# Performance work log

Measured on AMD Instinct MI355X. Metric: run time of the kernel, lower is better.

Reference implementation:

```python
import jax, jax.numpy as jnp
import numpy as np

B, T, D = 16, 2048, 256
QK = 64


def setup_inputs() -> dict:
    key = jax.random.key(0)
    ks = jax.random.split(key, 9)
    x = jax.random.normal(ks[0], (B, T, D), dtype=jnp.float32)
    sl = jax.random.uniform(ks[1], (B, T), dtype=jnp.float32)
    mask = jax.random.randint(ks[2], (B, T), 0, 2, dtype=jnp.int32)
    s = 1.0 / np.sqrt(D).astype(np.float32)
    Wq = jax.random.normal(ks[3], (QK, D), dtype=jnp.float32) * s
    bq = jnp.zeros((QK,), dtype=jnp.float32)
    Wk = jax.random.normal(ks[4], (QK, D), dtype=jnp.float32) * s
    bk = jnp.zeros((QK,), dtype=jnp.float32)
    Wv = jax.random.normal(ks[5], (D, D), dtype=jnp.float32) * s
    bv = jnp.zeros((D,), dtype=jnp.float32)
    return {"x": x, "sl": sl, "mask": mask, "Wq": Wq, "bq": bq,
            "Wk": Wk, "bk": bk, "Wv": Wv, "bv": bv}


def reference(x, sl, mask, Wq, bq, Wk, bk, Wv, bv):
    # x: [B,T,D], sl: [B,T] soft labels, mask: [B,T] valid positions
    sl = jnp.clip(sl, 0.0, 1.0)
    q = jnp.einsum('btd,ed->bte', x, Wq) + bq          # [B,T,QK]
    k = jnp.einsum('btd,ed->bte', x, Wk) + bk          # [B,T,QK]
    v = jnp.einsum('btd,ed->bte', x, Wv) + bv          # [B,T,D]
    scale = jnp.float32(1.0 / np.sqrt(QK))
    score = jnp.einsum('bte,bse->bts', q, k) * scale   # [B,T,T]
    # emotion scaling by (1 + sl_j^2) per key position j
    score = score * (1.0 + sl[:, None, :] ** 2)
    score = jnp.where(mask[:, None, :] == 0, jnp.float32(-1e9), score)
    prob = jax.nn.softmax(score, axis=-1)              # [B,T,T]
    out = jnp.einsum('bts,bsd->btd', prob, v)          # [B,T,D]
    return out.mean(axis=1)                            # [B,D]
```

## Files before the change

kernel.cpp:

```cpp
#include <hip/hip_runtime.h>
#include <hip/hip_bf16.h>
#include <stdint.h>

#define B_ 16
#define T_ 2048
#define D_ 256
#define QK_ 64
#define LOG2E 1.44269504088896340736f

typedef _Float16 f16;
typedef _Float16 f16x8 __attribute__((ext_vector_type(8)));
typedef float f32x16 __attribute__((ext_vector_type(16)));

__device__ __forceinline__ void gload_lds16(const void* g, void* l) {
    __builtin_amdgcn_global_load_lds(
        (const __attribute__((address_space(1))) uint32_t*)g,
        (__attribute__((address_space(3))) uint32_t*)l, 16, 0, 0);
}

__device__ __forceinline__ float fexp2(float x) {
#if __has_builtin(__builtin_amdgcn_exp2f)
    return __builtin_amdgcn_exp2f(x);
#else
    return exp2f(x);
#endif
}
__device__ __forceinline__ float flog2(float x) {
#if __has_builtin(__builtin_amdgcn_logf)
    return __builtin_amdgcn_logf(x);
#else
    return log2f(x);
#endif
}

__global__ __launch_bounds__(256) void wconv_kernel(
    const float* __restrict__ Wq, const float* __restrict__ Wk,
    f16* __restrict__ wh)
{
    const int i = blockIdx.x * 256 + threadIdx.x;
    const float v = (i < 64 * 256) ? Wq[i] : Wk[i - 64 * 256];
    wh[i] = (f16)v;
}

__global__ __launch_bounds__(256) void proj_mfma(
    const float* __restrict__ x, const float* __restrict__ sl,
    const f16* __restrict__ wh,
    const float* __restrict__ bq, const float* __restrict__ bk,
    f16* __restrict__ qh, f16* __restrict__ k2h)
{
    __shared__ __align__(16) f16 xs[64 * D_];
    __shared__ float ksc[64];
    const int b = blockIdx.y, t0 = blockIdx.x * 64;
    const int tid = threadIdx.x;
    const int wv = tid >> 6, l = tid & 63, lo = l & 31, hi = l >> 5;

    #pragma unroll
    for (int i = 0; i < 8; ++i) {
        const int f = i * 256 + tid;
        const int r = f >> 5, j = f & 31;
        const float* src = x + ((size_t)b * T_ + t0 + r) * D_ + j * 8;
        const float4 a0 = *(const float4*)src;
        const float4 a1 = *(const float4*)(src + 4);
        f16x8 h;
        h[0] = (f16)a0.x; h[1] = (f16)a0.y; h[2] = (f16)a0.z; h[3] = (f16)a0.w;
        h[4] = (f16)a1.x; h[5] = (f16)a1.y; h[6] = (f16)a1.z; h[7] = (f16)a1.w;
        *(f16x8*)(xs + r * D_ + ((j ^ (r & 31)) << 3)) = h;
    }
    if (tid < 64) {
        float s = sl[(size_t)b * T_ + t0 + tid];
        s = fminf(fmaxf(s, 0.f), 1.f);
        ksc[tid] = 0.125f * (1.f + s * s) * LOG2E;
    }
    __syncthreads();

    const int r0 = (wv & 1) * 32, c0 = (wv >> 1) * 64;
    f32x16 acc0, acc1;
    #pragma unroll
    for (int i = 0; i < 16; ++i) { acc0[i] = 0.f; acc1[i] = 0.f; }

    const int r = r0 + lo;
    const f16* wrow0 = wh + (size_t)(c0 + lo) * D_ + hi * 8;
    const f16* wrow1 = wh + (size_t)(c0 + 32 + lo) * D_ + hi * 8;
    #pragma unroll
    for (int ks = 0; ks < 16; ++ks) {
        const f16x8 a  = *(const f16x8*)(xs + r * D_ + ((((ks << 1) + hi) ^ (r & 31)) << 3));
        const f16x8 b0 = *(const f16x8*)(wrow0 + ks * 16);
        const f16x8 b1 = *(const f16x8*)(wrow1 + ks * 16);
        acc0 = __builtin_amdgcn_mfma_f32_32x32x16_f16(a, b0, acc0, 0, 0, 0);
        acc1 = __builtin_amdgcn_mfma_f32_32x32x16_f16(a, b1, acc1, 0, 0, 0);
    }

    __syncthreads();
    f16* hout = xs;
    {
        const int col0 = c0 + lo, col1 = c0 + 32 + lo;
        const float bias0 = (col0 < 64) ? bq[col0] : bk[col0 - 64];
        const float bias1 = (col1 < 64) ? bq[col1] : bk[col1 - 64];
        #pragma unroll
        for (int i = 0; i < 16; ++i) {
            const int row = r0 + (i & 3) + 8 * (i >> 2) + 4 * hi;
            float v0 = acc0[i] + bias0;
            float v1 = acc1[i] + bias1;
            if (col0 >= 64) v0 *= ksc[row];
            if (col1 >= 64) v1 *= ksc[row];
            hout[row * 128 + col0] = (f16)v0;
            hout[row * 128 + col1] = (f16)v1;
        }
    }
    __syncthreads();
    #pragma unroll
    for (int i = 0; i < 4; ++i) {
        const int f = i * 256 + tid;
        const int rr = f >> 4, j = f & 15;
        const f16x8 v = *(const f16x8*)(hout + rr * 128 + j * 8);
        if (j < 8) *(f16x8*)(qh  + ((size_t)b * T_ + t0 + rr) * QK_ + j * 8) = v;
        else       *(f16x8*)(k2h + ((size_t)b * T_ + t0 + rr) * QK_ + (j - 8) * 8) = v;
    }
}

__global__ __launch_bounds__(256) void z_part(
    const f16* __restrict__ qh, const f16* __restrict__ k2h,
    const int* __restrict__ mask, float* __restrict__ zpart)
{
    __shared__ __align__(16) f16 kt[2][128 * QK_];
    __shared__ float mv[2][128];
    const int b = blockIdx.y;
    const int t0 = (blockIdx.x & 15) * 128;
    const int ck = blockIdx.x >> 4;
    const int sbase = ck * 512;
    const int tid = threadIdx.x;
    const int wv = tid >> 6, l = tid & 63, lo = l & 31, hi = l >> 5;

    const f16* qrow = qh + (size_t)(b * T_ + t0 + wv * 32 + lo) * QK_;
    f16x8 a[4];
    #pragma unroll
    for (int kc = 0; kc < 4; ++kc)
        a[kc] = *(const f16x8*)(qrow + kc * 16 + hi * 8);

    float zp[16];
    #pragma unroll
    for (int i = 0; i < 16; ++i) zp[i] = 0.f;

    auto stage = [&](int s0, int buf) {
        const char* src = (const char*)(k2h + (size_t)(b * T_ + s0) * QK_);
        #pragma unroll
        for (int i = 0; i < 4; ++i) {
            const int o = wv * 4096 + i * 1024 + l * 16;
            const int r = o >> 7, jc = (o >> 4) & 7;
            gload_lds16(src + r * 128 + ((jc ^ (r & 7)) << 4),
                        (char*)kt[buf] + wv * 4096 + i * 1024);
        }
        if (tid < 128) mv[buf][tid] = mask[b * T_ + s0 + tid] ? 0.f : -1e9f;
    };

    stage(sbase, 0);
    __syncthreads();
    int cur = 0;
    #pragma unroll
    for (int it = 0; it < 4; ++it) {
        if (it + 1 < 4) stage(sbase + (it + 1) * 128, cur ^ 1);
        const f16* ktc = kt[cur];
        #pragma unroll
        for (int cg = 0; cg < 4; ++cg) {
            const int srow = cg * 32 + lo;
            const float mb = mv[cur][srow];
            f32x16 c;
            #pragma unroll
            for (int i = 0; i < 16; ++i) c[i] = mb;
            #pragma unroll
            for (int kc = 0; kc < 4; ++kc) {
                const int jcc = (kc * 2 + hi) ^ (srow & 7);
                const f16x8 bf = *(const f16x8*)((const char*)ktc + srow * 128 + (jcc << 4));
                c = __builtin_amdgcn_mfma_f32_32x32x16_f16(a[kc], bf, c, 0, 0, 0);
            }
            #pragma unroll
            for (int i = 0; i < 16; ++i) zp[i] += fexp2(c[i]);
        }
        __syncthreads();
        cur ^= 1;
    }

    #pragma unroll
    for (int off = 1; off <= 16; off <<= 1)
        #pragma unroll
        for (int i = 0; i < 16; ++i) zp[i] += __shfl_xor(zp[i], off);

    if (lo == 0) {
        #pragma unroll
        for (int i = 0; i < 16; ++i) {
            const int row = (i & 3) + 8 * (i >> 2) + 4 * hi;
            zpart[(size_t)(b * 4 + ck) * T_ + t0 + wv * 32 + row] = zp[i];
        }
    }
}

__global__ __launch_bounds__(256) void w_part(
    const f16* __restrict__ qh, const f16* __restrict__ k2h,
    const float* __restrict__ zpart, float* __restrict__ wpart)
{
    __shared__ __align__(16) f16 qt[2][128 * QK_];
    __shared__ float lz[2][128];
    const int b = blockIdx.y;
    const int s0b = (blockIdx.x & 15) * 128;
    const int tc = blockIdx.x >> 4;
    const int tbase = tc * 512;
    const int tid = threadIdx.x;
    const int wv = tid >> 6, l = tid & 63, lo = l & 31, hi = l >> 5;

    const f16* krow = k2h + (size_t)(b * T_ + s0b + wv * 32 + lo) * QK_;
    f16x8 a[4];
    #pragma unroll
    for (int kc = 0; kc < 4; ++kc)
        a[kc] = *(const f16x8*)(krow + kc * 16 + hi * 8);

    float wp[16];
    #pragma unroll
    for (int i = 0; i < 16; ++i) wp[i] = 0.f;

    auto stage = [&](int t0, int buf) {
        const char* src = (const char*)(qh + (size_t)(b * T_ + t0) * QK_);
        #pragma unroll
        for (int i = 0; i < 4; ++i) {
            const int o = wv * 4096 + i * 1024 + l * 16;
            const int r = o >> 7, jc = (o >> 4) & 7;
            gload_lds16(src + r * 128 + ((jc ^ (r & 7)) << 4),
                        (char*)qt[buf] + wv * 4096 + i * 1024);
        }
        if (tid < 128) {
            const float z = zpart[(size_t)(b * 4 + 0) * T_ + t0 + tid]
                          + zpart[(size_t)(b * 4 + 1) * T_ + t0 + tid]
                          + zpart[(size_t)(b * 4 + 2) * T_ + t0 + tid]
                          + zpart[(size_t)(b * 4 + 3) * T_ + t0 + tid];
            lz[buf][tid] = -flog2(z);
        }
    };

    stage(tbase, 0);
    __syncthreads();
    int cur = 0;
    #pragma unroll
    for (int it = 0; it < 4; ++it) {
        if (it + 1 < 4) stage(tbase + (it + 1) * 128, cur ^ 1);
        const f16* qtc = qt[cur];
        #pragma unroll
        for (int cg = 0; cg < 4; ++cg) {
            const int trow = cg * 32 + lo;
            const float bias = lz[cur][trow];
            f32x16 c;
            #pragma unroll
            for (int i = 0; i < 16; ++i) c[i] = bias;
            #pragma unroll
            for (int kc = 0; kc < 4; ++kc) {
                const int jcc = (kc * 2 + hi) ^ (trow & 7);
                const f16x8 bf = *(const f16x8*)((const char*)qtc + trow * 128 + (jcc << 4));
                c = __builtin_amdgcn_mfma_f32_32x32x16_f16(a[kc], bf, c, 0, 0, 0);
            }
            #pragma unroll
            for (int i = 0; i < 16; ++i) wp[i] += fexp2(c[i]);
        }
        __syncthreads();
        cur ^= 1;
    }

    #pragma unroll
    for (int off = 1; off <= 16; off <<= 1)
        #pragma unroll
        for (int i = 0; i < 16; ++i) wp[i] += __shfl_xor(wp[i], off);

    if (lo == 0) {
        #pragma unroll
        for (int i = 0; i < 16; ++i) {
            const int row = (i & 3) + 8 * (i >> 2) + 4 * hi;
            wpart[(size_t)(b * 4 + tc) * T_ + s0b + wv * 32 + row] = wp[i];
        }
    }
}

__global__ __launch_bounds__(256) void y_fused(
    const float* __restrict__ x, const float* __restrict__ wpart,
    const int* __restrict__ mask, float* __restrict__ ypart,
    float* __restrict__ swp)
{
    __shared__ float wloc[32];
    const int b  = blockIdx.y;
    const int ch = blockIdx.x;
    const int tid = threadIdx.x;

    if (tid < 32) {
        const int s = ch * 32 + tid;
        float v = wpart[(size_t)(b * 4 + 0) * T_ + s]
                + wpart[(size_t)(b * 4 + 1) * T_ + s]
                + wpart[(size_t)(b * 4 + 2) * T_ + s]
                + wpart[(size_t)(b * 4 + 3) * T_ + s];
        v *= mask[b * T_ + s] ? (1.f / (float)T_) : 0.f;
        wloc[tid] = v;
        float sv = v;
        #pragma unroll
        for (int off = 1; off <= 16; off <<= 1) sv += __shfl_xor(sv, off);
        if (tid == 0) swp[b * 64 + ch] = sv;
    }
    __syncthreads();

    const int d = tid;
    const float* xb = x + ((size_t)b * T_ + ch * 32) * D_;
    float acc = 0.f;
    #pragma unroll 8
    for (int s = 0; s < 32; ++s) acc += wloc[s] * xb[(size_t)s * D_ + d];
    ypart[((size_t)b * 64 + ch) * D_ + d] = acc;
}

__global__ __launch_bounds__(256) void outkernel(
    const float* __restrict__ ypart, const float* __restrict__ swp,
    const float* __restrict__ Wv, const float* __restrict__ bv,
    float* __restrict__ out)
{
    __shared__ __align__(16) float ys[D_];
    __shared__ float sw0;
    const int b   = blockIdx.x;
    const int tid = threadIdx.x;

    float yv = 0.f;
    #pragma unroll
    for (int ch = 0; ch < 64; ++ch) yv += ypart[((size_t)b * 64 + ch) * D_ + tid];
    ys[tid] = yv;

    float s = (tid < 64) ? swp[b * 64 + tid] : 0.f;
    #pragma unroll
    for (int off = 1; off <= 32; off <<= 1) s += __shfl_xor(s, off);
    if (tid == 0) sw0 = s;
    __syncthreads();

    const float sw = sw0;
    const float4* wv4 = (const float4*)(Wv + (size_t)tid * D_);
    const float4* ys4 = (const float4*)ys;
    float o = 0.f;
    for (int i = 0; i < D_ / 4; ++i) {
        const float4 a = wv4[i];
        const float4 y = ys4[i];
        o += a.x * y.x + a.y * y.y + a.z * y.z + a.w * y.w;
    }
    out[(size_t)b * D_ + tid] = o + bv[tid] * sw;
}

extern "C" void kernel_launch(void* const* d_in, const int* in_sizes, int n_in,
                              void* d_out, int out_size, void* d_ws, size_t ws_size,
                              hipStream_t stream)
{
    const float* x    = (const float*)d_in[0];
    const float* sl   = (const float*)d_in[1];
    const int*   mask = (const int*)d_in[2];
    const float* Wq   = (const float*)d_in[3];
    const float* bq   = (const float*)d_in[4];
    const float* Wk   = (const float*)d_in[5];
    const float* bk   = (const float*)d_in[6];
    const float* Wv   = (const float*)d_in[7];
    const float* bv   = (const float*)d_in[8];
    float* out = (float*)d_out;

    f16*   qh    = (f16*)d_ws;
    f16*   k2h   = qh + (size_t)B_ * T_ * QK_;
    f16*   wh    = k2h + (size_t)B_ * T_ * QK_;
    float* zpart = (float*)(wh + 128 * D_);
    float* wpart = zpart + (size_t)B_ * 4 * T_;
    float* swp   = wpart + (size_t)B_ * 4 * T_;
    float* yp    = swp + B_ * 64;

    wconv_kernel<<<dim3(128), 256, 0, stream>>>(Wq, Wk, wh);
    proj_mfma  <<<dim3(T_ / 64, B_), 256, 0, stream>>>(x, sl, wh, bq, bk, qh, k2h);
    z_part     <<<dim3(64, B_), 256, 0, stream>>>(qh, k2h, mask, zpart);
    w_part     <<<dim3(64, B_), 256, 0, stream>>>(qh, k2h, zpart, wpart);
    y_fused    <<<dim3(64, B_), 256, 0, stream>>>(x, wpart, mask, yp, swp);
    outkernel  <<<dim3(B_), 256, 0, stream>>>(yp, swp, Wv, bv, out);
}
```

Measured before the change: 81.31 us.

## Drop LDS staging in projection and score kernels, load operands directly from global

The projection kernel now handles 32 rows per block. Each wave loads its x rows from global memory, converts them to fp16 with packed conversion, and feeds them straight into MFMA, so the shared-memory x tile and one barrier are gone. The z_part and w_part kernels drop their double-buffered LDS staging of K/Q tiles and mask/normaliser values. Each lane now reads its B-operand rows and mask/log-sum values directly from global (L2-cached) memory, which removes the barriers and LDS traffic. The cost is more redundant global loads per wave and more reliance on cache hits, and the projection grid doubles in size.

```diff
diff --git a/kernel.cpp b/kernel.cpp
--- a/kernel.cpp
+++ b/kernel.cpp
@@ -9,14 +9,10 @@
 #define LOG2E 1.44269504088896340736f
 
 typedef _Float16 f16;
+typedef _Float16 f16x2 __attribute__((ext_vector_type(2)));
+typedef __fp16 fp16x2 __attribute__((ext_vector_type(2)));
 typedef _Float16 f16x8 __attribute__((ext_vector_type(8)));
 typedef float f32x16 __attribute__((ext_vector_type(16)));
-
-__device__ __forceinline__ void gload_lds16(const void* g, void* l) {
-    __builtin_amdgcn_global_load_lds(
-        (const __attribute__((address_space(1))) uint32_t*)g,
-        (__attribute__((address_space(3))) uint32_t*)l, 16, 0, 0);
-}
 
 __device__ __forceinline__ float fexp2(float x) {
 #if __has_builtin(__builtin_amdgcn_exp2f)
@@ -32,6 +28,14 @@
     return log2f(x);
 #endif
 }
+__device__ __forceinline__ f16x2 cvt2(float a, float b) {
+#if __has_builtin(__builtin_amdgcn_cvt_pkrtz)
+    fp16x2 r = __builtin_amdgcn_cvt_pkrtz(a, b);
+    return __builtin_bit_cast(f16x2, r);
+#else
+    f16x2 r; r[0] = (f16)a; r[1] = (f16)b; return r;
+#endif
+}
 
 __global__ __launch_bounds__(256) void wconv_kernel(
     const float* __restrict__ Wq, const float* __restrict__ Wk,
@@ -48,73 +52,55 @@
     const float* __restrict__ bq, const float* __restrict__ bk,
     f16* __restrict__ qh, f16* __restrict__ k2h)
 {
-    __shared__ __align__(16) f16 xs[64 * D_];
-    __shared__ float ksc[64];
-    const int b = blockIdx.y, t0 = blockIdx.x * 64;
+    __shared__ __align__(16) f16 hout[32 * 128];
+    __shared__ float ksc[32];
+    const int b = blockIdx.y, t0 = blockIdx.x * 32;
     const int tid = threadIdx.x;
     const int wv = tid >> 6, l = tid & 63, lo = l & 31, hi = l >> 5;
 
-    #pragma unroll
-    for (int i = 0; i < 8; ++i) {
-        const int f = i * 256 + tid;
-        const int r = f >> 5, j = f & 31;
-        const float* src = x + ((size_t)b * T_ + t0 + r) * D_ + j * 8;
-        const float4 a0 = *(const float4*)src;
-        const float4 a1 = *(const float4*)(src + 4);
-        f16x8 h;
-        h[0] = (f16)a0.x; h[1] = (f16)a0.y; h[2] = (f16)a0.z; h[3] = (f16)a0.w;
-        h[4] = (f16)a1.x; h[5] = (f16)a1.y; h[6] = (f16)a1.z; h[7] = (f16)a1.w;
-        *(f16x8*)(xs + r * D_ + ((j ^ (r & 31)) << 3)) = h;
-    }
-    if (tid < 64) {
+    if (tid < 32) {
         float s = sl[(size_t)b * T_ + t0 + tid];
         s = fminf(fmaxf(s, 0.f), 1.f);
         ksc[tid] = 0.125f * (1.f + s * s) * LOG2E;
     }
+
+    const int c0 = wv * 32;
+    const float* xrow = x + (size_t)(b * T_ + t0 + lo) * D_ + hi * 8;
+    const f16*  wrow  = wh + (size_t)(c0 + lo) * D_ + hi * 8;
+
+    f32x16 acc;
+    #pragma unroll
+    for (int i = 0; i < 16; ++i) acc[i] = 0.f;
+
+    #pragma unroll
+    for (int ks = 0; ks < 16; ++ks) {
+        const float4 a0 = *(const float4*)(xrow + ks * 16);
+        const float4 a1 = *(const float4*)(xrow + ks * 16 + 4);
+        union { f16x2 h2[4]; f16x8 h8; } u;
+        u.h2[0] = cvt2(a0.x, a0.y); u.h2[1] = cvt2(a0.z, a0.w);
+        u.h2[2] = cvt2(a1.x, a1.y); u.h2[3] = cvt2(a1.z, a1.w);
+        const f16x8 bf = *(const f16x8*)(wrow + ks * 16);
+        acc = __builtin_amdgcn_mfma_f32_32x32x16_f16(u.h8, bf, acc, 0, 0, 0);
+    }
+
+    const int e = c0 + lo;
+    const float bias = (e < 64) ? bq[e] : bk[e - 64];
     __syncthreads();
-
-    const int r0 = (wv & 1) * 32, c0 = (wv >> 1) * 64;
-    f32x16 acc0, acc1;
-    #pragma unroll
-    for (int i = 0; i < 16; ++i) { acc0[i] = 0.f; acc1[i] = 0.f; }
-
-    const int r = r0 + lo;
-    const f16* wrow0 = wh + (size_t)(c0 + lo) * D_ + hi * 8;
-    const f16* wrow1 = wh + (size_t)(c0 + 32 + lo) * D_ + hi * 8;
-    #pragma unroll
-    for (int ks = 0; ks < 16; ++ks) {
-        const f16x8 a  = *(const f16x8*)(xs + r * D_ + ((((ks << 1) + hi) ^ (r & 31)) << 3));
-        const f16x8 b0 = *(const f16x8*)(wrow0 + ks * 16);
-        const f16x8 b1 = *(const f16x8*)(wrow1 + ks * 16);
-        acc0 = __builtin_amdgcn_mfma_f32_32x32x16_f16(a, b0, acc0, 0, 0, 0);
-        acc1 = __builtin_amdgcn_mfma_f32_32x32x16_f16(a, b1, acc1, 0, 0, 0);
-    }
-
+    #pragma unroll
+    for (int i = 0; i < 16; ++i) {
+        const int row = (i & 3) + 8 * (i >> 2) + 4 * hi;
+        float v = acc[i] + bias;
+        if (e >= 64) v *= ksc[row];
+        hout[row * 128 + e] = (f16)v;
+    }
     __syncthreads();
-    f16* hout = xs;
-    {
-        const int col0 = c0 + lo, col1 = c0 + 32 + lo;
-        const float bias0 = (col0 < 64) ? bq[col0] : bk[col0 - 64];
-        const float bias1 = (col1 < 64) ? bq[col1] : bk[col1 - 64];
-        #pragma unroll
-        for (int i = 0; i < 16; ++i) {
-            const int row = r0 + (i & 3) + 8 * (i >> 2) + 4 * hi;
-            float v0 = acc0[i] + bias0;
-            float v1 = acc1[i] + bias1;
-            if (col0 >= 64) v0 *= ksc[row];
-            if (col1 >= 64) v1 *= ksc[row];
-            hout[row * 128 + col0] = (f16)v0;
-            hout[row * 128 + col1] = (f16)v1;
-        }
-    }
-    __syncthreads();
-    #pragma unroll
-    for (int i = 0; i < 4; ++i) {
+    #pragma unroll
+    for (int i = 0; i < 2; ++i) {
         const int f = i * 256 + tid;
         const int rr = f >> 4, j = f & 15;
         const f16x8 v = *(const f16x8*)(hout + rr * 128 + j * 8);
-        if (j < 8) *(f16x8*)(qh  + ((size_t)b * T_ + t0 + rr) * QK_ + j * 8) = v;
-        else       *(f16x8*)(k2h + ((size_t)b * T_ + t0 + rr) * QK_ + (j - 8) * 8) = v;
+        if (j < 8) *(f16x8*)(qh  + (size_t)(b * T_ + t0 + rr) * QK_ + j * 8) = v;
+        else       *(f16x8*)(k2h + (size_t)(b * T_ + t0 + rr) * QK_ + (j - 8) * 8) = v;
     }
 }
 
@@ -122,8 +108,6 @@
     const f16* __restrict__ qh, const f16* __restrict__ k2h,
     const int* __restrict__ mask, float* __restrict__ zpart)
 {
-    __shared__ __align__(16) f16 kt[2][128 * QK_];
-    __shared__ float mv[2][128];
     const int b = blockIdx.y;
     const int t0 = (blockIdx.x & 15) * 128;
     const int ck = blockIdx.x >> 4;
@@ -131,53 +115,32 @@
     const int tid = threadIdx.x;
     const int wv = tid >> 6, l = tid & 63, lo = l & 31, hi = l >> 5;
 
-    const f16* qrow = qh + (size_t)(b * T_ + t0 + wv * 32 + lo) * QK_;
+    const f16* qrow = qh + (size_t)(b * T_ + t0 + wv * 32 + lo) * QK_ + hi * 8;
     f16x8 a[4];
     #pragma unroll
-    for (int kc = 0; kc < 4; ++kc)
-        a[kc] = *(const f16x8*)(qrow + kc * 16 + hi * 8);
+    for (int kc = 0; kc < 4; ++kc) a[kc] = *(const f16x8*)(qrow + kc * 16);
 
     float zp[16];
     #pragma unroll
     for (int i = 0; i < 16; ++i) zp[i] = 0.f;
 
-    auto stage = [&](int s0, int buf) {
-        const char* src = (const char*)(k2h + (size_t)(b * T_ + s0) * QK_);
-        #pragma unroll
-        for (int i = 0; i < 4; ++i) {
-            const int o = wv * 4096 + i * 1024 + l * 16;
-            const int r = o >> 7, jc = (o >> 4) & 7;
-            gload_lds16(src + r * 128 + ((jc ^ (r & 7)) << 4),
-                        (char*)kt[buf] + wv * 4096 + i * 1024);
+    const f16* kbase = k2h + (size_t)(b * T_) * QK_ + hi * 8;
+    const int* mbase = mask + b * T_;
+
+    for (int g = 0; g < 16; ++g) {
+        const int scol = sbase + g * 32 + lo;
+        const float mb = mbase[scol] ? 0.f : -1e9f;
+        f32x16 c;
+        #pragma unroll
+        for (int i = 0; i < 16; ++i) c[i] = mb;
+        const f16* kr = kbase + (size_t)scol * QK_;
+        #pragma unroll
+        for (int kc = 0; kc < 4; ++kc) {
+            const f16x8 bf = *(const f16x8*)(kr + kc * 16);
+            c = __builtin_amdgcn_mfma_f32_32x32x16_f16(a[kc], bf, c, 0, 0, 0);
         }
-        if (tid < 128) mv[buf][tid] = mask[b * T_ + s0 + tid] ? 0.f : -1e9f;
-    };
-
-    stage(sbase, 0);
-    __syncthreads();
-    int cur = 0;
-    #pragma unroll
-    for (int it = 0; it < 4; ++it) {
-        if (it + 1 < 4) stage(sbase + (it + 1) * 128, cur ^ 1);
-        const f16* ktc = kt[cur];
-        #pragma unroll
-        for (int cg = 0; cg < 4; ++cg) {
-            const int srow = cg * 32 + lo;
-            const float mb = mv[cur][srow];
-            f32x16 c;
-            #pragma unroll
-            for (int i = 0; i < 16; ++i) c[i] = mb;
-            #pragma unroll
-            for (int kc = 0; kc < 4; ++kc) {
-                const int jcc = (kc * 2 + hi) ^ (srow & 7);
-                const f16x8 bf = *(const f16x8*)((const char*)ktc + srow * 128 + (jcc << 4));
-                c = __builtin_amdgcn_mfma_f32_32x32x16_f16(a[kc], bf, c, 0, 0, 0);
-            }
-            #pragma unroll
-            for (int i = 0; i < 16; ++i) zp[i] += fexp2(c[i]);
-        }
-        __syncthreads();
-        cur ^= 1;
+        #pragma unroll
+        for (int i = 0; i < 16; ++i) zp[i] += fexp2(c[i]);
     }
 
     #pragma unroll
@@ -198,8 +161,6 @@
     const f16* __restrict__ qh, const f16* __restrict__ k2h,
     const float* __restrict__ zpart, float* __restrict__ wpart)
 {
-    __shared__ __align__(16) f16 qt[2][128 * QK_];
-    __shared__ float lz[2][128];
     const int b = blockIdx.y;
     const int s0b = (blockIdx.x & 15) * 128;
     const int tc = blockIdx.x >> 4;
@@ -207,59 +168,33 @@
     const int tid = threadIdx.x;
     const int wv = tid >> 6, l = tid & 63, lo = l & 31, hi = l >> 5;
 
-    const f16* krow = k2h + (size_t)(b * T_ + s0b + wv * 32 + lo) * QK_;
+    const f16* krow = k2h + (size_t)(b * T_ + s0b + wv * 32 + lo) * QK_ + hi * 8;
     f16x8 a[4];
     #pragma unroll
-    for (int kc = 0; kc < 4; ++kc)
-        a[kc] = *(const f16x8*)(krow + kc * 16 + hi * 8);
+    for (int kc = 0; kc < 4; ++kc) a[kc] = *(const f16x8*)(krow + kc * 16);
 
     float wp[16];
     #pragma unroll
     for (int i = 0; i < 16; ++i) wp[i] = 0.f;
 
-    auto stage = [&](int t0, int buf) {
-        const char* src = (const char*)(qh + (size_t)(b * T_ + t0) * QK_);
-        #pragma unroll
-        for (int i = 0; i < 4; ++i) {
-            const int o = wv * 4096 + i * 1024 + l * 16;
-            const int r = o >> 7, jc = (o >> 4) & 7;
-            gload_lds16(src + r * 128 + ((jc ^ (r & 7)) << 4),
-                        (char*)qt[buf] + wv * 4096 + i * 1024);
+    const f16* qbase = qh + (size_t)(b * T_) * QK_ + hi * 8;
+    const float* zb = zpart + (size_t)(b * 4) * T_;
+
+    for (int g = 0; g < 16; ++g) {
+        const int tcol = tbase + g * 32 + lo;
+        const float z = zb[tcol] + zb[T_ + tcol] + zb[2 * T_ + tcol] + zb[3 * T_ + tcol];
+        const float lz = -flog2(z);
+        f32x16 c;
+        #pragma unroll
+        for (int i = 0; i < 16; ++i) c[i] = lz;
+        const f16* qr = qbase + (size_t)tcol * QK_;
+        #pragma unroll
+        for (int kc = 0; kc < 4; ++kc) {
+            const f16x8 bf = *(const f16x8*)(qr + kc * 16);
+            c = __builtin_amdgcn_mfma_f32_32x32x16_f16(a[kc], bf, c, 0, 0, 0);
         }
-        if (tid < 128) {
-            const float z = zpart[(size_t)(b * 4 + 0) * T_ + t0 + tid]
-                          + zpart[(size_t)(b * 4 + 1) * T_ + t0 + tid]
-                          + zpart[(size_t)(b * 4 + 2) * T_ + t0 + tid]
-                          + zpart[(size_t)(b * 4 + 3) * T_ + t0 + tid];
-            lz[buf][tid] = -flog2(z);
-        }
-    };
-
-    stage(tbase, 0);
-    __syncthreads();
-    int cur = 0;
-    #pragma unroll
-    for (int it = 0; it < 4; ++it) {
-        if (it + 1 < 4) stage(tbase + (it + 1) * 128, cur ^ 1);
-        const f16* qtc = qt[cur];
-        #pragma unroll
-        for (int cg = 0; cg < 4; ++cg) {
-            const int trow = cg * 32 + lo;
-            const float bias = lz[cur][trow];
-            f32x16 c;
-            #pragma unroll
-            for (int i = 0; i < 16; ++i) c[i] = bias;
-            #pragma unroll
-            for (int kc = 0; kc < 4; ++kc) {
-                const int jcc = (kc * 2 + hi) ^ (trow & 7);
-                const f16x8 bf = *(const f16x8*)((const char*)qtc + trow * 128 + (jcc << 4));
-                c = __builtin_amdgcn_mfma_f32_32x32x16_f16(a[kc], bf, c, 0, 0, 0);
-            }
-            #pragma unroll
-            for (int i = 0; i < 16; ++i) wp[i] += fexp2(c[i]);
-        }
-        __syncthreads();
-        cur ^= 1;
+        #pragma unroll
+        for (int i = 0; i < 16; ++i) wp[i] += fexp2(c[i]);
     }
 
     #pragma unroll
@@ -366,7 +301,7 @@
     float* yp    = swp + B_ * 64;
 
     wconv_kernel<<<dim3(128), 256, 0, stream>>>(Wq, Wk, wh);
-    proj_mfma  <<<dim3(T_ / 64, B_), 256, 0, stream>>>(x, sl, wh, bq, bk, qh, k2h);
+    proj_mfma  <<<dim3(T_ / 32, B_), 256, 0, stream>>>(x, sl, wh, bq, bk, qh, k2h);
     z_part     <<<dim3(64, B_), 256, 0, stream>>>(qh, k2h, mask, zpart);
     w_part     <<<dim3(64, B_), 256, 0, stream>>>(qh, k2h, zpart, wpart);
     y_fused    <<<dim3(64, B_), 256, 0, stream>>>(x, wpart, mask, yp, swp);
```

New measurement: 121.8 us. +49.8%, slower.
